# Optimization experiments

Hardware: AMD Instinct MI355X
Metric: run time of the kernel (lower is better)

## Reference

```python
import jax, jax.numpy as jnp
import numpy as np

KERNEL = 3
PAD = 1


def setup_inputs() -> dict:
    key = jax.random.key(0)
    kx, kw = jax.random.split(key)
    x = jax.random.normal(kx, (4, 64, 512, 512), dtype=jnp.float32)
    weights = jax.random.uniform(kw, (64, KERNEL, KERNEL), dtype=jnp.float32)
    return {"x": x, "weights": weights}


def reference(x, weights):
    # Morphological dilation (max-plus conv): for each output pixel,
    # max over the kxk window of (x + w). Equivalent to the torch module's
    # unfold -> elementwise add of broadcast weights -> max over k*k,
    # but computed with shifted slices so the im2col tensor is never built.
    B, C, H, W = x.shape
    k, p = KERNEL, PAD
    Ho = H + 2 * p - k + 1
    Wo = W + 2 * p - k + 1
    # nn.Unfold zero-pads, so pad with zeros (not -inf) to stay faithful.
    xp = jnp.pad(x, ((0, 0), (0, 0), (p, p), (p, p)))
    out = None
    for i in range(k):  # fixed small kernel loop (9 iters), fully vectorized inside
        for j in range(k):
            patch = xp[:, :, i:i + Ho, j:j + Wo] + weights[None, :, i, j, None, None]
            out = patch if out is None else jnp.maximum(out, patch)
    # compute_max views as [B, C, k*k, L] and maxes over dim 2 -> [B, C, L]
    return out.reshape(B, C, Ho * Wo)
```

## Files before the change

### kernel.cpp

```cpp
#include <hip/hip_runtime.h>


#define BB 4
#define CC 64
#define HH 512
#define WW 512
#define W4 (WW / 4)
#define RB 4
#define HB (HH / RB)

typedef float vfloat4 __attribute__((ext_vector_type(4)));

__global__ __launch_bounds__(256) void morph_dilate_kernel(
    const float* __restrict__ x,
    const float* __restrict__ wts,
    float* __restrict__ out) {
    int tid = blockIdx.x * blockDim.x + threadIdx.x;
    int wi    = tid & (W4 - 1);
    int w4    = wi * 4;
    int hb    = (tid >> 7) & (HB - 1);
    int h0    = hb * RB;
    int plane = tid >> 14;
    int c     = plane & (CC - 1);

    const float* xplane = x + (size_t)plane * (HH * WW);
    const float* wt = wts + c * 9;

    float w00 = wt[0], w01 = wt[1], w02 = wt[2];
    float w10 = wt[3], w11 = wt[4], w12 = wt[5];
    float w20 = wt[6], w21 = wt[7], w22 = wt[8];

    float v[6][6];
#pragma unroll
    for (int i = 0; i < 6; ++i) {
        int r = h0 - 1 + i;
        if (r >= 0 && r < HH) {
            const float* xrow = xplane + r * WW;
            v[i][0] = (w4 > 0) ? xrow[w4 - 1] : 0.0f;
            vfloat4 mid = *reinterpret_cast<const vfloat4*>(xrow + w4);
            v[i][1] = mid.x; v[i][2] = mid.y; v[i][3] = mid.z; v[i][4] = mid.w;
            v[i][5] = (w4 + 4 < WW) ? xrow[w4 + 4] : 0.0f;
        } else {
#pragma unroll
            for (int j = 0; j < 6; ++j) v[i][j] = 0.0f;
        }
    }

    float* oplane = out + (size_t)plane * (HH * WW);
#pragma unroll
    for (int rt = 0; rt < RB; ++rt) {
        vfloat4 o;
#pragma unroll
        for (int t = 0; t < 4; ++t) {
            float m;
            m =          v[rt + 0][t + 0] + w00;
            m = fmaxf(m, v[rt + 0][t + 1] + w01);
            m = fmaxf(m, v[rt + 0][t + 2] + w02);
            m = fmaxf(m, v[rt + 1][t + 0] + w10);
            m = fmaxf(m, v[rt + 1][t + 1] + w11);
            m = fmaxf(m, v[rt + 1][t + 2] + w12);
            m = fmaxf(m, v[rt + 2][t + 0] + w20);
            m = fmaxf(m, v[rt + 2][t + 1] + w21);
            m = fmaxf(m, v[rt + 2][t + 2] + w22);
            o[t] = m;
        }
        *reinterpret_cast<vfloat4*>(oplane + (size_t)(h0 + rt) * WW + w4) = o;
    }
}

extern "C" void kernel_launch(void* const* d_in, const int* in_sizes, int n_in,
                              void* d_out, int out_size, void* d_ws, size_t ws_size,
                              hipStream_t stream) {
    const float* x   = (const float*)d_in[0];
    const float* wts = (const float*)d_in[1];
    float* out = (float*)d_out;

    int total_threads = BB * CC * HB * W4;
    int block = 256;
    int grid = total_threads / block;
    morph_dilate_kernel<<<grid, block, 0, stream>>>(x, wts, out);
}
```

Before: 421.4 us.

## Use wavefront shuffles for halo columns and process eight rows per thread

Each thread now computes eight output rows instead of four, which cuts the redundant halo row reads from 6/4 to 10/8 per output row. The per-row scalar loads of the left and right neighbour columns are replaced by cross-lane shuffles of the adjacent lane's float4, and only the first and last lanes of a wave load their edge element from memory. The cost is higher register pressure, half as many threads, and extra shuffle instructions. The kernel is memory-bound, so the gain depends on how many redundant loads the L1/L2 caches were already absorbing.

```diff
diff --git a/kernel.cpp b/kernel.cpp
--- a/kernel.cpp
+++ b/kernel.cpp
@@ -6,7 +6,7 @@
 #define HH 512
 #define WW 512
 #define W4 (WW / 4)
-#define RB 4
+#define RB 8
 #define HB (HH / RB)
 
 typedef float vfloat4 __attribute__((ext_vector_type(4)));
@@ -20,8 +20,9 @@
     int w4    = wi * 4;
     int hb    = (tid >> 7) & (HB - 1);
     int h0    = hb * RB;
-    int plane = tid >> 14;
+    int plane = tid >> 13;
     int c     = plane & (CC - 1);
+    int lane  = threadIdx.x & 63;
 
     const float* xplane = x + (size_t)plane * (HH * WW);
     const float* wt = wts + c * 9;
@@ -30,38 +31,52 @@
     float w10 = wt[3], w11 = wt[4], w12 = wt[5];
     float w20 = wt[6], w21 = wt[7], w22 = wt[8];
 
-    float v[6][6];
+    bool isl = (lane == 0);
+    bool isr = (lane == 63);
+    int ecol = isl ? (w4 - 1) : (w4 + 4);
+    bool eneed = (isl && w4 > 0) || (isr && w4 + 4 < WW);
+
+    float vm[10][4];
+    float vl[10], vr[10];
 #pragma unroll
-    for (int i = 0; i < 6; ++i) {
+    for (int i = 0; i < 10; ++i) {
         int r = h0 - 1 + i;
         if (r >= 0 && r < HH) {
             const float* xrow = xplane + r * WW;
-            v[i][0] = (w4 > 0) ? xrow[w4 - 1] : 0.0f;
             vfloat4 mid = *reinterpret_cast<const vfloat4*>(xrow + w4);
-            v[i][1] = mid.x; v[i][2] = mid.y; v[i][3] = mid.z; v[i][4] = mid.w;
-            v[i][5] = (w4 + 4 < WW) ? xrow[w4 + 4] : 0.0f;
+            float edge = 0.0f;
+            if (eneed) edge = xrow[ecol];
+            float l = __shfl_up(mid.w, 1);
+            float rgt = __shfl_down(mid.x, 1);
+            if (isl) l = edge;
+            if (isr) rgt = edge;
+            vm[i][0] = mid.x; vm[i][1] = mid.y; vm[i][2] = mid.z; vm[i][3] = mid.w;
+            vl[i] = l; vr[i] = rgt;
         } else {
-#pragma unroll
-            for (int j = 0; j < 6; ++j) v[i][j] = 0.0f;
+            vm[i][0] = vm[i][1] = vm[i][2] = vm[i][3] = 0.0f;
+            vl[i] = vr[i] = 0.0f;
         }
     }
 
     float* oplane = out + (size_t)plane * (HH * WW);
 #pragma unroll
     for (int rt = 0; rt < RB; ++rt) {
+        float a0[6] = {vl[rt],     vm[rt][0],     vm[rt][1],     vm[rt][2],     vm[rt][3],     vr[rt]};
+        float a1[6] = {vl[rt + 1], vm[rt + 1][0], vm[rt + 1][1], vm[rt + 1][2], vm[rt + 1][3], vr[rt + 1]};
+        float a2[6] = {vl[rt + 2], vm[rt + 2][0], vm[rt + 2][1], vm[rt + 2][2], vm[rt + 2][3], vr[rt + 2]};
         vfloat4 o;
 #pragma unroll
         for (int t = 0; t < 4; ++t) {
             float m;
-            m =          v[rt + 0][t + 0] + w00;
-            m = fmaxf(m, v[rt + 0][t + 1] + w01);
-            m = fmaxf(m, v[rt + 0][t + 2] + w02);
-            m = fmaxf(m, v[rt + 1][t + 0] + w10);
-            m = fmaxf(m, v[rt + 1][t + 1] + w11);
-            m = fmaxf(m, v[rt + 1][t + 2] + w12);
-            m = fmaxf(m, v[rt + 2][t + 0] + w20);
-            m = fmaxf(m, v[rt + 2][t + 1] + w21);
-            m = fmaxf(m, v[rt + 2][t + 2] + w22);
+            m =          a0[t + 0] + w00;
+            m = fmaxf(m, a0[t + 1] + w01);
+            m = fmaxf(m, a0[t + 2] + w02);
+            m = fmaxf(m, a1[t + 0] + w10);
+            m = fmaxf(m, a1[t + 1] + w11);
+            m = fmaxf(m, a1[t + 2] + w12);
+            m = fmaxf(m, a2[t + 0] + w20);
+            m = fmaxf(m, a2[t + 1] + w21);
+            m = fmaxf(m, a2[t + 2] + w22);
             o[t] = m;
         }
         *reinterpret_cast<vfloat4*>(oplane + (size_t)(h0 + rt) * WW + w4) = o;
```

Result: slower. 436.0 us (+3.5%).
